# Performance work log

Measured on AMD Instinct MI355X. Metric: run time of the kernel, lower is better.

The kernel has to match this reference:

```python
import jax, jax.numpy as jnp
import numpy as np
from jax import lax

B, T, D = 8, 4096, 512

def setup_inputs() -> dict:
    key = jax.random.key(0)
    k0, k1, k2 = jax.random.split(key, 3)
    x = jax.random.normal(k0, (B, T, D), dtype=jnp.float32)
    # transform: Linear(2D, 2D) -> GELU -> Linear(2D, D)
    W1 = jax.random.normal(k1, (2 * D, 2 * D), dtype=jnp.float32) * 0.02
    b1 = jnp.zeros((2 * D,), dtype=jnp.float32)
    W2 = jax.random.normal(k2, (D, 2 * D), dtype=jnp.float32) * 0.02
    b2 = jnp.zeros((D,), dtype=jnp.float32)
    return {"x": x, "W1": W1, "b1": b1, "W2": W2, "b2": b2}

def reference(x, W1, b1, W2, b2):
    # x: [B, T, D]. Sequential gated memory update over T, vectorized over B.
    Bb, Tt, Dd = x.shape

    def step(mem, xt):
        # mem, xt: [B, D]
        edge = jnp.concatenate([xt, mem], axis=-1)          # [B, 2D]
        h = jax.nn.gelu(edge @ W1.T + b1, approximate=False)  # exact GELU (torch default)
        proposed = h @ W2.T + b2                             # [B, D]
        g = jax.nn.sigmoid(proposed)
        mem = mem * (1.0 - g) + proposed * g
        return mem, mem

    xs = jnp.swapaxes(x, 0, 1)                               # [T, B, D]
    mem0 = jnp.zeros((Bb, Dd), dtype=x.dtype)
    _, ys = lax.scan(step, mem0, xs)                         # ys: [T, B, D]
    return jnp.swapaxes(ys, 0, 1)                            # [B, T, D]
```

## Files before the change

### kernel.cpp

```cpp
#include <hip/hip_runtime.h>
#include <cmath>

typedef __attribute__((ext_vector_type(4))) float f32x4;
typedef __attribute__((ext_vector_type(8))) short s16x8;
typedef __attribute__((ext_vector_type(4))) short s16x4;
typedef unsigned long long u64;

#define TSTEPS 4096
#define NCU 32

__device__ __forceinline__ short f2bf(float f) {
  unsigned u = __float_as_uint(f);
  unsigned r = (u + 0x7FFFu + ((u >> 16) & 1u)) >> 16;
  return (short)r;
}
__device__ __forceinline__ float bf2f(short s) {
  return __uint_as_float(((unsigned)(unsigned short)s) << 16);
}

__global__ void __launch_bounds__(256) pre_gemm(
    const float* __restrict__ x, const float* __restrict__ W1,
    const float* __restrict__ b1, float* __restrict__ pre1)
{
  __shared__ float As[16][136];
  __shared__ float Bs[16][136];
  const int tid = threadIdx.x;
  const int m0 = blockIdx.x * 128, j0 = blockIdx.y * 128;
  const int r = tid >> 1, half = tid & 1;
  const int tx = tid & 15, ty = tid >> 4;

  float acc[8][8];
#pragma unroll
  for (int a = 0; a < 8; a++)
#pragma unroll
    for (int b = 0; b < 8; b++) acc[a][b] = 0.f;

  const int row = m0 + r;
  const float* xrow = x + (((size_t)(row & 7) * 4096) + (size_t)(row >> 3)) * 512;
  const float* wrow = W1 + (size_t)(j0 + r) * 1024;

  for (int k0 = 0; k0 < 512; k0 += 16) {
    f32x4 a0 = *(const f32x4*)(xrow + k0 + half * 8);
    f32x4 a1 = *(const f32x4*)(xrow + k0 + half * 8 + 4);
    f32x4 w0 = *(const f32x4*)(wrow + k0 + half * 8);
    f32x4 w1 = *(const f32x4*)(wrow + k0 + half * 8 + 4);
    __syncthreads();
#pragma unroll
    for (int q = 0; q < 4; q++) {
      As[half * 8 + q][r] = a0[q];
      As[half * 8 + 4 + q][r] = a1[q];
      Bs[half * 8 + q][r] = w0[q];
      Bs[half * 8 + 4 + q][r] = w1[q];
    }
    __syncthreads();
#pragma unroll
    for (int kk = 0; kk < 16; kk++) {
      f32x4 ra0 = *(const f32x4*)&As[kk][ty * 8];
      f32x4 ra1 = *(const f32x4*)&As[kk][ty * 8 + 4];
      f32x4 rb0 = *(const f32x4*)&Bs[kk][tx * 8];
      f32x4 rb1 = *(const f32x4*)&Bs[kk][tx * 8 + 4];
#pragma unroll
      for (int a = 0; a < 4; a++)
#pragma unroll
        for (int b = 0; b < 4; b++) {
          acc[a][b]         += ra0[a] * rb0[b];
          acc[a][b + 4]     += ra0[a] * rb1[b];
          acc[a + 4][b]     += ra1[a] * rb0[b];
          acc[a + 4][b + 4] += ra1[a] * rb1[b];
        }
    }
  }
  float bias[8];
#pragma unroll
  for (int b = 0; b < 8; b++) bias[b] = b1[j0 + tx * 8 + b];
#pragma unroll
  for (int a = 0; a < 8; a++) {
    float* dst = pre1 + (size_t)(m0 + ty * 8 + a) * 1024 + j0 + tx * 8;
    f32x4 v0, v1;
#pragma unroll
    for (int b = 0; b < 4; b++) { v0[b] = acc[a][b] + bias[b]; v1[b] = acc[a][b + 4] + bias[b + 4]; }
    *(f32x4*)dst = v0;
    *(f32x4*)(dst + 4) = v1;
  }
}

__global__ void __launch_bounds__(256) seq_scan(
    const float* __restrict__ W1, const float* __restrict__ W2,
    const float* __restrict__ b2, const float* __restrict__ pre1,
    float* __restrict__ out, float* __restrict__ accbuf,
    unsigned* __restrict__ bar, unsigned* __restrict__ rel)
{
  const int c = blockIdx.x;
  const int tid = threadIdx.x;
  const int l = tid & 63;
  const int w = tid >> 6;

  extern __shared__ char lds[];
  short* w1bh = (short*)lds;
  short* w1bl = w1bh + 32 * 520;
  short* w2h  = w1bl + 32 * 520;
  short* w2l  = w2h + 512 * 36;
  short* memh = w2l + 512 * 36;
  short* meml = memh + 9 * 520;
  short* hh   = meml + 9 * 520;
  short* hl   = hh + 9 * 40;
  float* scr  = (float*)(hl + 9 * 40);

  for (int e = tid; e < 32 * 128; e += 256) {
    int jl = e >> 7, k4 = (e & 127) << 2;
    f32x4 v = *(const f32x4*)(W1 + (size_t)(c * 32 + jl) * 1024 + 512 + k4);
#pragma unroll
    for (int q = 0; q < 4; q++) {
      short hi = f2bf(v[q]);
      w1bh[jl * 520 + k4 + q] = hi;
      w1bl[jl * 520 + k4 + q] = f2bf(v[q] - bf2f(hi));
    }
  }
  for (int e = tid; e < 512 * 8; e += 256) {
    int i = e >> 3, j4 = (e & 7) << 2;
    f32x4 v = *(const f32x4*)(W2 + (size_t)i * 1024 + c * 32 + j4);
#pragma unroll
    for (int q = 0; q < 4; q++) {
      short hi = f2bf(v[q]);
      w2h[i * 36 + j4 + q] = hi;
      w2l[i * 36 + j4 + q] = f2bf(v[q] - bf2f(hi));
    }
  }
  for (int e = tid; e < 9 * 520; e += 256) { memh[e] = 0; meml[e] = 0; }
  for (int e = tid; e < 9 * 40; e += 256)  { hh[e] = 0; hl[e] = 0; }

  const int mg = tid >> 5;
  const int i0own = (tid & 31) * 16;
  float memr[16];
  float b2r[16];
#pragma unroll
  for (int q = 0; q < 16; q++) { memr[q] = 0.f; b2r[q] = b2[i0own + q]; }

  const int jt = w & 1, kh = w >> 1;
  const int jg = c * 32 + jt * 16 + (l & 15);
  const int m_ep = (l >> 4) * 4;
  const bool ep = (w < 2) && (l < 32);
  float p1r[4];
  if (ep) {
#pragma unroll
    for (int rr = 0; rr < 4; rr++) p1r[rr] = pre1[(size_t)(0 * 8 + m_ep + rr) * 1024 + jg];
  }

  const int arow = ((l & 15) < 8) ? (l & 15) : 8;
  const int aoff = arow * 520 + (l >> 4) * 8;
  const int boff = (jt * 16 + (l & 15)) * 520 + (l >> 4) * 8;
  const int haoff = arow * 40 + (l >> 4) * 8;

  __syncthreads();

  for (int t = 0; t < TSTEPS; t++) {
    {
      f32x4 a0 = {0.f,0.f,0.f,0.f}, a1 = a0, a2 = a0;
#pragma unroll
      for (int ks = 0; ks < 8; ks++) {
        const int ko = kh * 256 + ks * 32;
        s16x8 ah = *(const s16x8*)(memh + aoff + ko);
        s16x8 al = *(const s16x8*)(meml + aoff + ko);
        s16x8 bh = *(const s16x8*)(w1bh + boff + ko);
        s16x8 bl = *(const s16x8*)(w1bl + boff + ko);
        a0 = __builtin_amdgcn_mfma_f32_16x16x32_bf16(ah, bh, a0, 0, 0, 0);
        a1 = __builtin_amdgcn_mfma_f32_16x16x32_bf16(al, bh, a1, 0, 0, 0);
        a2 = __builtin_amdgcn_mfma_f32_16x16x32_bf16(ah, bl, a2, 0, 0, 0);
      }
      f32x4 acc = a0 + a1 + a2;
      if (w >= 2) *(f32x4*)(scr + (w - 2) * 256 + l * 4) = acc;
      __syncthreads();
      if (w < 2) {
        acc += *(const f32x4*)(scr + w * 256 + l * 4);
        if (l < 32) {
#pragma unroll
          for (int rr = 0; rr < 4; rr++) {
            float xv = acc[rr] + p1r[rr];
            float hv = 0.5f * xv * (1.0f + erff(xv * 0.70710678118654752f));
            short hhi = f2bf(hv);
            hh[(m_ep + rr) * 40 + jt * 16 + (l & 15)] = hhi;
            hl[(m_ep + rr) * 40 + jt * 16 + (l & 15)] = f2bf(hv - bf2f(hhi));
          }
        }
      }
    }
    __syncthreads();

    {
      float* accw = accbuf + (size_t)(t & 3) * 4096;
      s16x8 ha = *(const s16x8*)(hh + haoff);
      s16x8 hb = *(const s16x8*)(hl + haoff);
      const int n0 = w * 128;
#pragma unroll
      for (int tt = 0; tt < 8; tt++) {
        const int tl = (tt + c) & 7;
        const int icol = n0 + tl * 16 + (l & 15);
        const int woff = icol * 36 + (l >> 4) * 8;
        s16x8 bh, bl;
        *(s16x4*)&bh = *(const s16x4*)(w2h + woff);
        *((s16x4*)&bh + 1) = *(const s16x4*)(w2h + woff + 4);
        *(s16x4*)&bl = *(const s16x4*)(w2l + woff);
        *((s16x4*)&bl + 1) = *(const s16x4*)(w2l + woff + 4);
        f32x4 p0 = {0.f,0.f,0.f,0.f}, p1 = p0, p2 = p0;
        p0 = __builtin_amdgcn_mfma_f32_16x16x32_bf16(ha, bh, p0, 0, 0, 0);
        p1 = __builtin_amdgcn_mfma_f32_16x16x32_bf16(hb, bh, p1, 0, 0, 0);
        p2 = __builtin_amdgcn_mfma_f32_16x16x32_bf16(ha, bl, p2, 0, 0, 0);
        f32x4 p = p0 + p1 + p2;
        if (l < 32) {
          const int mrow = (l >> 4) * 4;
#pragma unroll
          for (int rr = 0; rr < 4; rr++)
            atomicAdd(accw + ((mrow + rr) << 9) + icol, p[rr]);
        }
      }
    }

    if (tid < 64) {
      u64* z = (u64*)(accbuf + (size_t)((t + 2) & 3) * 4096);
      __hip_atomic_store(z + c * 64 + tid, 0ull, __ATOMIC_RELAXED, __HIP_MEMORY_SCOPE_AGENT);
    }

    if (ep && t + 1 < TSTEPS) {
#pragma unroll
      for (int rr = 0; rr < 4; rr++)
        p1r[rr] = pre1[(size_t)((t + 1) * 8 + m_ep + rr) * 1024 + jg];
    }

    __syncthreads();
    if (tid == 0) {
      unsigned old = __hip_atomic_fetch_add(bar, 1u, __ATOMIC_RELAXED, __HIP_MEMORY_SCOPE_AGENT);
      if (old == (unsigned)(NCU * (t + 1) - 1)) {
        __hip_atomic_store(rel, (unsigned)(t + 1), __ATOMIC_RELAXED, __HIP_MEMORY_SCOPE_AGENT);
      } else {
        while (__hip_atomic_load(rel, __ATOMIC_RELAXED, __HIP_MEMORY_SCOPE_AGENT) < (unsigned)(t + 1)) {}
      }
    }
    __syncthreads();

    {
      const u64* av = (const u64*)(accbuf + (size_t)(t & 3) * 4096);
      u64 vals[8];
#pragma unroll
      for (int q8 = 0; q8 < 8; q8++)
        vals[q8] = __hip_atomic_load(av + tid * 8 + q8, __ATOMIC_RELAXED, __HIP_MEMORY_SCOPE_AGENT);
      float nmv[16];
#pragma unroll
      for (int q8 = 0; q8 < 8; q8++) {
#pragma unroll
        for (int hlf = 0; hlf < 2; hlf++) {
          const int q = 2 * q8 + hlf;
          float v = __uint_as_float((unsigned)(hlf ? (vals[q8] >> 32) : vals[q8]));
          float prop = v + b2r[q];
          float g = 1.0f / (1.0f + __expf(-prop));
          float nm = memr[q] + g * (prop - memr[q]);
          memr[q] = nm;
          nmv[q] = nm;
        }
      }
      s16x8 vh0, vl0, vh1, vl1;
#pragma unroll
      for (int q = 0; q < 8; q++) {
        short hi = f2bf(nmv[q]);
        vh0[q] = hi; vl0[q] = f2bf(nmv[q] - bf2f(hi));
        short hi2 = f2bf(nmv[q + 8]);
        vh1[q] = hi2; vl1[q] = f2bf(nmv[q + 8] - bf2f(hi2));
      }
      *(s16x8*)(memh + mg * 520 + i0own) = vh0;
      *(s16x8*)(memh + mg * 520 + i0own + 8) = vh1;
      *(s16x8*)(meml + mg * 520 + i0own) = vl0;
      *(s16x8*)(meml + mg * 520 + i0own + 8) = vl1;
      if ((tid & 31) == c) {
        float* op = out + ((size_t)mg * TSTEPS + t) * 512 + i0own;
#pragma unroll
        for (int q4 = 0; q4 < 4; q4++) {
          f32x4 v;
#pragma unroll
          for (int j = 0; j < 4; j++) v[j] = nmv[q4 * 4 + j];
          *(f32x4*)(op + q4 * 4) = v;
        }
      }
    }
    __syncthreads();
  }
}

extern "C" void kernel_launch(void* const* d_in, const int* in_sizes, int n_in,
                              void* d_out, int out_size, void* d_ws, size_t ws_size,
                              hipStream_t stream) {
  const float* x  = (const float*)d_in[0];
  const float* W1 = (const float*)d_in[1];
  const float* b1 = (const float*)d_in[2];
  const float* W2 = (const float*)d_in[3];
  const float* b2 = (const float*)d_in[4];
  float* out = (float*)d_out;
  char* ws = (char*)d_ws;

  float*    accbuf = (float*)(ws + 0);
  unsigned* bar    = (unsigned*)(ws + 65536);
  unsigned* rel    = (unsigned*)(ws + 65664);
  float*    pre1   = (float*)(ws + (1u << 20));

  hipMemsetAsync(ws, 0, 65792, stream);

  dim3 gp(256, 8);
  pre_gemm<<<gp, dim3(256), 0, stream>>>(x, W1, b1, pre1);

  const int LDS_BYTES = 162496;
  hipFuncSetAttribute((const void*)seq_scan,
                      hipFuncAttributeMaxDynamicSharedMemorySize, LDS_BYTES);
  seq_scan<<<dim3(NCU), dim3(256), LDS_BYTES, stream>>>(
      W1, W2, b2, pre1, out, accbuf, bar, rel);
}
```

Baseline: 19.49 ms.

## Shard atomic accumulators, use per-wave barrier counters, relayout pre1 for coalesced loads

The W2 partial-sum atomics are split across four shard buffers (selected by block index) so fewer blocks contend on the same addresses, and readers sum the four shards. The single-thread grid barrier with a release flag is replaced by four per-wave counters that every thread polls directly, which removes the block-level __syncthreads around the barrier. pre1 is written in a per-timestep, per-block contiguous layout so the scan's prefetch is more local, and that prefetch now runs after the barrier. The cost is four times the accbuf reads per step plus heavier polling traffic on the counters.

```diff
diff --git a/kernel.cpp b/kernel.cpp
--- a/kernel.cpp
+++ b/kernel.cpp
@@ -17,6 +17,7 @@
 __device__ __forceinline__ float bf2f(short s) {
   return __uint_as_float(((unsigned)(unsigned short)s) << 16);
 }
+__device__ __forceinline__ unsigned umin2(unsigned a, unsigned b) { return a < b ? a : b; }
 
 __global__ void __launch_bounds__(256) pre_gemm(
     const float* __restrict__ x, const float* __restrict__ W1,
@@ -73,14 +74,18 @@
   float bias[8];
 #pragma unroll
   for (int b = 0; b < 8; b++) bias[b] = b1[j0 + tx * 8 + b];
+
+  const int tt = (m0 >> 3) + ty;
+  const int col0 = j0 + tx * 8;
+  const int c2 = col0 >> 5, jl0 = col0 & 31;
+  float* dst = pre1 + (size_t)tt * 8192 + (size_t)c2 * 256 + jl0;
 #pragma unroll
   for (int a = 0; a < 8; a++) {
-    float* dst = pre1 + (size_t)(m0 + ty * 8 + a) * 1024 + j0 + tx * 8;
     f32x4 v0, v1;
 #pragma unroll
     for (int b = 0; b < 4; b++) { v0[b] = acc[a][b] + bias[b]; v1[b] = acc[a][b + 4] + bias[b + 4]; }
-    *(f32x4*)dst = v0;
-    *(f32x4*)(dst + 4) = v1;
+    *(f32x4*)(dst + a * 32) = v0;
+    *(f32x4*)(dst + a * 32 + 4) = v1;
   }
 }
 
@@ -88,7 +93,7 @@
     const float* __restrict__ W1, const float* __restrict__ W2,
     const float* __restrict__ b2, const float* __restrict__ pre1,
     float* __restrict__ out, float* __restrict__ accbuf,
-    unsigned* __restrict__ bar, unsigned* __restrict__ rel)
+    unsigned* __restrict__ bar)
 {
   const int c = blockIdx.x;
   const int tid = threadIdx.x;
@@ -137,19 +142,20 @@
   for (int q = 0; q < 16; q++) { memr[q] = 0.f; b2r[q] = b2[i0own + q]; }
 
   const int jt = w & 1, kh = w >> 1;
-  const int jg = c * 32 + jt * 16 + (l & 15);
   const int m_ep = (l >> 4) * 4;
   const bool ep = (w < 2) && (l < 32);
+  const float* p1base = pre1 + (size_t)c * 256 + m_ep * 32 + jt * 16 + (l & 15);
   float p1r[4];
   if (ep) {
 #pragma unroll
-    for (int rr = 0; rr < 4; rr++) p1r[rr] = pre1[(size_t)(0 * 8 + m_ep + rr) * 1024 + jg];
+    for (int rr = 0; rr < 4; rr++) p1r[rr] = p1base[rr * 32];
   }
 
   const int arow = ((l & 15) < 8) ? (l & 15) : 8;
   const int aoff = arow * 520 + (l >> 4) * 8;
   const int boff = (jt * 16 + (l & 15)) * 520 + (l >> 4) * 8;
   const int haoff = arow * 40 + (l >> 4) * 8;
+  const int shard = c & 3;
 
   __syncthreads();
 
@@ -187,7 +193,7 @@
     __syncthreads();
 
     {
-      float* accw = accbuf + (size_t)(t & 3) * 4096;
+      float* accw = accbuf + ((size_t)(t & 3) * 4 + shard) * 4096;
       s16x8 ha = *(const s16x8*)(hh + haoff);
       s16x8 hb = *(const s16x8*)(hl + haoff);
       const int n0 = w * 128;
@@ -215,41 +221,56 @@
       }
     }
 
-    if (tid < 64) {
-      u64* z = (u64*)(accbuf + (size_t)((t + 2) & 3) * 4096);
-      __hip_atomic_store(z + c * 64 + tid, 0ull, __ATOMIC_RELAXED, __HIP_MEMORY_SCOPE_AGENT);
-    }
-
-    if (ep && t + 1 < TSTEPS) {
-#pragma unroll
-      for (int rr = 0; rr < 4; rr++)
-        p1r[rr] = pre1[(size_t)((t + 1) * 8 + m_ep + rr) * 1024 + jg];
-    }
-
-    __syncthreads();
-    if (tid == 0) {
-      unsigned old = __hip_atomic_fetch_add(bar, 1u, __ATOMIC_RELAXED, __HIP_MEMORY_SCOPE_AGENT);
-      if (old == (unsigned)(NCU * (t + 1) - 1)) {
-        __hip_atomic_store(rel, (unsigned)(t + 1), __ATOMIC_RELAXED, __HIP_MEMORY_SCOPE_AGENT);
-      } else {
-        while (__hip_atomic_load(rel, __ATOMIC_RELAXED, __HIP_MEMORY_SCOPE_AGENT) < (unsigned)(t + 1)) {}
-      }
-    }
-    __syncthreads();
-
-    {
-      const u64* av = (const u64*)(accbuf + (size_t)(t & 3) * 4096);
-      u64 vals[8];
-#pragma unroll
-      for (int q8 = 0; q8 < 8; q8++)
-        vals[q8] = __hip_atomic_load(av + tid * 8 + q8, __ATOMIC_RELAXED, __HIP_MEMORY_SCOPE_AGENT);
+    __builtin_amdgcn_sched_barrier(0);
+    __builtin_amdgcn_s_waitcnt(0);
+    __builtin_amdgcn_sched_barrier(0);
+    if (l == 0)
+      __hip_atomic_fetch_add(bar + w * 32, 1u, __ATOMIC_RELAXED, __HIP_MEMORY_SCOPE_AGENT);
+
+    {
+      u64* z = (u64*)accbuf + (size_t)((t + 2) & 3) * 8192 + c * 256 + tid;
+      __hip_atomic_store(z, 0ull, __ATOMIC_RELAXED, __HIP_MEMORY_SCOPE_AGENT);
+    }
+
+    {
+      const unsigned target = (unsigned)(NCU * (t + 1));
+      while (true) {
+        unsigned b0 = __hip_atomic_load(bar + 0,  __ATOMIC_RELAXED, __HIP_MEMORY_SCOPE_AGENT);
+        unsigned b1 = __hip_atomic_load(bar + 32, __ATOMIC_RELAXED, __HIP_MEMORY_SCOPE_AGENT);
+        unsigned b2_ = __hip_atomic_load(bar + 64, __ATOMIC_RELAXED, __HIP_MEMORY_SCOPE_AGENT);
+        unsigned b3 = __hip_atomic_load(bar + 96, __ATOMIC_RELAXED, __HIP_MEMORY_SCOPE_AGENT);
+        if (umin2(umin2(b0, b1), umin2(b2_, b3)) >= target) break;
+      }
+      __builtin_amdgcn_sched_barrier(0);
+    }
+
+    {
+      const u64* av = (const u64*)accbuf + (size_t)(t & 3) * 8192;
+      const int base = mg * 256 + (tid & 31) * 8;
+      u64 vals[4][8];
+#pragma unroll
+      for (int s = 0; s < 4; s++)
+#pragma unroll
+        for (int q8 = 0; q8 < 8; q8++)
+          vals[s][q8] = __hip_atomic_load(av + s * 2048 + base + q8,
+                                          __ATOMIC_RELAXED, __HIP_MEMORY_SCOPE_AGENT);
+      if (ep && t + 1 < TSTEPS) {
+        const float* pb = p1base + (size_t)(t + 1) * 8192;
+#pragma unroll
+        for (int rr = 0; rr < 4; rr++) p1r[rr] = pb[rr * 32];
+      }
       float nmv[16];
 #pragma unroll
       for (int q8 = 0; q8 < 8; q8++) {
 #pragma unroll
         for (int hlf = 0; hlf < 2; hlf++) {
           const int q = 2 * q8 + hlf;
-          float v = __uint_as_float((unsigned)(hlf ? (vals[q8] >> 32) : vals[q8]));
+          float v = 0.f;
+#pragma unroll
+          for (int s = 0; s < 4; s++) {
+            u64 x8 = vals[s][q8];
+            v += __uint_as_float((unsigned)(hlf ? (x8 >> 32) : x8));
+          }
           float prop = v + b2r[q];
           float g = 1.0f / (1.0f + __expf(-prop));
           float nm = memr[q] + g * (prop - memr[q]);
@@ -296,11 +317,10 @@
   char* ws = (char*)d_ws;
 
   float*    accbuf = (float*)(ws + 0);
-  unsigned* bar    = (unsigned*)(ws + 65536);
-  unsigned* rel    = (unsigned*)(ws + 65664);
-  float*    pre1   = (float*)(ws + (1u << 20));
-
-  hipMemsetAsync(ws, 0, 65792, stream);
+  unsigned* bar    = (unsigned*)(ws + 262144);
+  float*    pre1   = (float*)(ws + (1u << 21));
+
+  hipMemsetAsync(ws, 0, 262144 + 512, stream);
 
   dim3 gp(256, 8);
   pre_gemm<<<gp, dim3(256), 0, stream>>>(x, W1, b1, pre1);
@@ -309,5 +329,5 @@
   hipFuncSetAttribute((const void*)seq_scan,
                       hipFuncAttributeMaxDynamicSharedMemorySize, LDS_BYTES);
   seq_scan<<<dim3(NCU), dim3(256), LDS_BYTES, stream>>>(
-      W1, W2, b2, pre1, out, accbuf, bar, rel);
-}
+      W1, W2, b2, pre1, out, accbuf, bar);
+}
```

Result: slower. 42.60 ms (+118.6%).

## Simplify grid barrier, relayout pre1 per-CU, use LDS-only barriers

Applied to the files above, without the earlier changes.

Replaces the two-phase grid barrier (atomic counter plus separate release flag) with a single monotonic counter that every block increments and polls. The arrive now happens before the buffer zeroing and the pre1 prefetch, so that work overlaps the wait. pre1 is rewritten in a per-timestep, per-CU layout so each block reads contiguous data. Intra-block __syncthreads calls that only guard LDS become s_waitcnt lgkmcnt plus s_barrier, so they no longer wait on outstanding global memory operations. The risk is memory-ordering subtlety: relaxed atomics and an LDS-only wait must still publish the atomicAdd partial sums before other blocks read them.

```diff
diff --git a/kernel.cpp b/kernel.cpp
--- a/kernel.cpp
+++ b/kernel.cpp
@@ -16,6 +16,13 @@
 }
 __device__ __forceinline__ float bf2f(short s) {
   return __uint_as_float(((unsigned)(unsigned short)s) << 16);
+}
+
+__device__ __forceinline__ void bar_lds() {
+  __builtin_amdgcn_sched_barrier(0);
+  asm volatile("s_waitcnt lgkmcnt(0)" ::: "memory");
+  __builtin_amdgcn_s_barrier();
+  __builtin_amdgcn_sched_barrier(0);
 }
 
 __global__ void __launch_bounds__(256) pre_gemm(
@@ -73,14 +80,18 @@
   float bias[8];
 #pragma unroll
   for (int b = 0; b < 8; b++) bias[b] = b1[j0 + tx * 8 + b];
+
+  const int tt = (m0 >> 3) + ty;
+  const int col0 = j0 + tx * 8;
+  const int c2 = col0 >> 5, jl0 = col0 & 31;
+  float* dst = pre1 + (size_t)tt * 8192 + (size_t)c2 * 256 + jl0;
 #pragma unroll
   for (int a = 0; a < 8; a++) {
-    float* dst = pre1 + (size_t)(m0 + ty * 8 + a) * 1024 + j0 + tx * 8;
     f32x4 v0, v1;
 #pragma unroll
     for (int b = 0; b < 4; b++) { v0[b] = acc[a][b] + bias[b]; v1[b] = acc[a][b + 4] + bias[b + 4]; }
-    *(f32x4*)dst = v0;
-    *(f32x4*)(dst + 4) = v1;
+    *(f32x4*)(dst + a * 32) = v0;
+    *(f32x4*)(dst + a * 32 + 4) = v1;
   }
 }
 
@@ -88,7 +99,7 @@
     const float* __restrict__ W1, const float* __restrict__ W2,
     const float* __restrict__ b2, const float* __restrict__ pre1,
     float* __restrict__ out, float* __restrict__ accbuf,
-    unsigned* __restrict__ bar, unsigned* __restrict__ rel)
+    unsigned* __restrict__ bar)
 {
   const int c = blockIdx.x;
   const int tid = threadIdx.x;
@@ -137,13 +148,13 @@
   for (int q = 0; q < 16; q++) { memr[q] = 0.f; b2r[q] = b2[i0own + q]; }
 
   const int jt = w & 1, kh = w >> 1;
-  const int jg = c * 32 + jt * 16 + (l & 15);
   const int m_ep = (l >> 4) * 4;
   const bool ep = (w < 2) && (l < 32);
+  const float* p1base = pre1 + (size_t)c * 256 + m_ep * 32 + jt * 16 + (l & 15);
   float p1r[4];
   if (ep) {
 #pragma unroll
-    for (int rr = 0; rr < 4; rr++) p1r[rr] = pre1[(size_t)(0 * 8 + m_ep + rr) * 1024 + jg];
+    for (int rr = 0; rr < 4; rr++) p1r[rr] = p1base[rr * 32];
   }
 
   const int arow = ((l & 15) < 8) ? (l & 15) : 8;
@@ -169,7 +180,7 @@
       }
       f32x4 acc = a0 + a1 + a2;
       if (w >= 2) *(f32x4*)(scr + (w - 2) * 256 + l * 4) = acc;
-      __syncthreads();
+      bar_lds();
       if (w < 2) {
         acc += *(const f32x4*)(scr + w * 256 + l * 4);
         if (l < 32) {
@@ -184,7 +195,7 @@
         }
       }
     }
-    __syncthreads();
+    bar_lds();
 
     {
       float* accw = accbuf + (size_t)(t & 3) * 4096;
@@ -215,30 +226,29 @@
       }
     }
 
+    __syncthreads();
+    if (tid == 0)
+      __hip_atomic_fetch_add(bar, 1u, __ATOMIC_RELAXED, __HIP_MEMORY_SCOPE_AGENT);
+
     if (tid < 64) {
-      u64* z = (u64*)(accbuf + (size_t)((t + 2) & 3) * 4096);
-      __hip_atomic_store(z + c * 64 + tid, 0ull, __ATOMIC_RELAXED, __HIP_MEMORY_SCOPE_AGENT);
+      u64* z = (u64*)accbuf + (size_t)((t + 2) & 3) * 2048 + c * 64 + tid;
+      __hip_atomic_store(z, 0ull, __ATOMIC_RELAXED, __HIP_MEMORY_SCOPE_AGENT);
     }
 
     if (ep && t + 1 < TSTEPS) {
-#pragma unroll
-      for (int rr = 0; rr < 4; rr++)
-        p1r[rr] = pre1[(size_t)((t + 1) * 8 + m_ep + rr) * 1024 + jg];
-    }
-
+      const float* pb = p1base + (size_t)(t + 1) * 8192;
+#pragma unroll
+      for (int rr = 0; rr < 4; rr++) p1r[rr] = pb[rr * 32];
+    }
+
+    if (tid == 0) {
+      const unsigned target = (unsigned)(NCU * (t + 1));
+      while (__hip_atomic_load(bar, __ATOMIC_RELAXED, __HIP_MEMORY_SCOPE_AGENT) < target) {}
+    }
     __syncthreads();
-    if (tid == 0) {
-      unsigned old = __hip_atomic_fetch_add(bar, 1u, __ATOMIC_RELAXED, __HIP_MEMORY_SCOPE_AGENT);
-      if (old == (unsigned)(NCU * (t + 1) - 1)) {
-        __hip_atomic_store(rel, (unsigned)(t + 1), __ATOMIC_RELAXED, __HIP_MEMORY_SCOPE_AGENT);
-      } else {
-        while (__hip_atomic_load(rel, __ATOMIC_RELAXED, __HIP_MEMORY_SCOPE_AGENT) < (unsigned)(t + 1)) {}
-      }
-    }
-    __syncthreads();
 
     {
-      const u64* av = (const u64*)(accbuf + (size_t)(t & 3) * 4096);
+      const u64* av = (const u64*)accbuf + (size_t)(t & 3) * 2048;
       u64 vals[8];
 #pragma unroll
       for (int q8 = 0; q8 < 8; q8++)
@@ -280,7 +290,7 @@
         }
       }
     }
-    __syncthreads();
+    bar_lds();
   }
 }
 
@@ -297,10 +307,9 @@
 
   float*    accbuf = (float*)(ws + 0);
   unsigned* bar    = (unsigned*)(ws + 65536);
-  unsigned* rel    = (unsigned*)(ws + 65664);
   float*    pre1   = (float*)(ws + (1u << 20));
 
-  hipMemsetAsync(ws, 0, 65792, stream);
+  hipMemsetAsync(ws, 0, 65536 + 256, stream);
 
   dim3 gp(256, 8);
   pre_gemm<<<gp, dim3(256), 0, stream>>>(x, W1, b1, pre1);
@@ -309,5 +318,5 @@
   hipFuncSetAttribute((const void*)seq_scan,
                       hipFuncAttributeMaxDynamicSharedMemorySize, LDS_BYTES);
   seq_scan<<<dim3(NCU), dim3(256), LDS_BYTES, stream>>>(
-      W1, W2, b2, pre1, out, accbuf, bar, rel);
-}
+      W1, W2, b2, pre1, out, accbuf, bar);
+}
```

Result: no change. 19.28 ms (-1.1%).
